# Performance work log

Measured on AMD Instinct MI355X. Metric: run time of the kernel, lower is better.

## Reference

```python
import jax, jax.numpy as jnp
import numpy as np

DECAY = 0.99
EPS = 1e-05
TEMP = 1.0


def setup_inputs() -> dict:
    key = jax.random.key(0)
    k1, k2, k3 = jax.random.split(key, 3)
    B, T, D, C = 64, 512, 256, 1024
    x = jax.random.normal(k1, (B, T, D), dtype=jnp.float32)
    embed = jax.random.normal(k2, (1, C, D), dtype=jnp.float32)
    embed_avg = jax.random.normal(k3, (1, C, D), dtype=jnp.float32)
    cluster_size = jnp.ones((1, C), dtype=jnp.float32)
    return {"x": x, "embed": embed, "embed_avg": embed_avg, "cluster_size": cluster_size}


def reference(x, embed, embed_avg, cluster_size):
    B, T, D = x.shape
    H, C, _ = embed.shape  # H = num_codebooks = 1
    flatten = x.reshape(H, B * T, D)  # pack_one 'h * d'
    e = jax.lax.stop_gradient(embed)  # learnable_codebook = False

    dist = (2.0 * jnp.einsum('hnd,hcd->hnc', flatten, e)
            - jnp.sum(flatten * flatten, axis=-1, keepdims=True)
            - jnp.sum(e * e, axis=-1)[:, None, :])  # [h, N, C]

    # gumbel_sample: deterministic argmax + straight-through one-hot
    embed_ind = jnp.argmax(dist, axis=-1)  # [h, N]
    probs = jax.nn.softmax(dist / TEMP, axis=-1)
    hard = jax.nn.one_hot(embed_ind, C, dtype=dist.dtype)
    embed_onehot = probs + jax.lax.stop_gradient(hard - probs)  # [h, N, C]

    # quantize via onehot matmul (training path)
    quantize = jnp.einsum('hnc,hcd->hnd', embed_onehot, e).reshape(B, T, D)

    # EMA codebook update
    cs_new = DECAY * cluster_size + (1.0 - DECAY) * embed_onehot.sum(axis=1)  # [h, C]
    embed_sum = jnp.einsum('hnd,hnc->hcd', flatten, embed_onehot)  # [h, C, D]
    ea_new = DECAY * embed_avg + (1.0 - DECAY) * embed_sum
    n = jnp.sum(cs_new, axis=-1, keepdims=True)
    cs_smoothed = (cs_new + EPS) / (n + C * EPS) * n  # laplace smoothing * n
    embed_norm = ea_new / cs_smoothed[..., None]  # new codebook [h, C, D]

    return (quantize, embed_ind.reshape(B, T), embed_norm, cs_new)
```

## Files before the change

### kernel.cpp

```cpp
#include <hip/hip_runtime.h>
#include <cstdint>

#define DECAY 0.99f
#define OMD   0.01f
#define EPSV  1e-5f

constexpr int N_PTS   = 32768;
constexpr int D_DIM   = 256;
constexpr int C_CODES = 1024;
constexpr int KPACK   = 768;

constexpr int PG = 4;
constexpr int PK = 8;
constexpr int LCAP = 8192;

typedef _Float16 half8  __attribute__((ext_vector_type(8)));
typedef _Float16 half4v __attribute__((ext_vector_type(4)));
typedef float    floatx4 __attribute__((ext_vector_type(4)));

constexpr size_t WS_ENORM = 0;
constexpr size_t WS_CSSUM = 1024;
constexpr size_t WS_PCNT  = 2048;
constexpr size_t WS_CAND  = 8192;
constexpr size_t WS_A16   = WS_CAND + 1048576;
constexpr size_t WS_B16   = WS_A16 + 12582912;
constexpr size_t WS_TOTAL_FLOATS = WS_B16 + 393216;

__device__ __forceinline__ void async_copy16(const void* g, void* s) {
    __builtin_amdgcn_global_load_lds(
        (const __attribute__((address_space(1))) unsigned int*)(uintptr_t)g,
        (__attribute__((address_space(3))) unsigned int*)(uintptr_t)s, 16, 0, 0);
}

__global__ __launch_bounds__(256) void vq_prep_x(const float* __restrict__ X,
                                                 _Float16* __restrict__ A) {
    int i = blockIdx.x * 256 + threadIdx.x;
    int n = i >> 6, kq = (i & 63) * 4;
    float4 v = reinterpret_cast<const float4*>(X)[i];
    _Float16 h0 = (_Float16)v.x, h1 = (_Float16)v.y, h2 = (_Float16)v.z, h3 = (_Float16)v.w;
    _Float16 l0 = (_Float16)(v.x - (float)h0), l1 = (_Float16)(v.y - (float)h1);
    _Float16 l2 = (_Float16)(v.z - (float)h2), l3 = (_Float16)(v.w - (float)h3);
    half4v hi = {h0, h1, h2, h3};
    half4v lo = {l0, l1, l2, l3};
    _Float16* row = A + (size_t)n * KPACK;
    *reinterpret_cast<half4v*>(row + kq)       = hi;
    *reinterpret_cast<half4v*>(row + 256 + kq) = hi;
    *reinterpret_cast<half4v*>(row + 512 + kq) = lo;
}

__global__ __launch_bounds__(256) void vq_prep_e(const float* __restrict__ E,
                                                 _Float16* __restrict__ B) {
    int i = blockIdx.x * 256 + threadIdx.x;
    int c = i >> 6, kq = (i & 63) * 4;
    float4 v = reinterpret_cast<const float4*>(E)[i];
    _Float16 h0 = (_Float16)v.x, h1 = (_Float16)v.y, h2 = (_Float16)v.z, h3 = (_Float16)v.w;
    _Float16 l0 = (_Float16)(v.x - (float)h0), l1 = (_Float16)(v.y - (float)h1);
    _Float16 l2 = (_Float16)(v.z - (float)h2), l3 = (_Float16)(v.w - (float)h3);
    half4v hi = {h0, h1, h2, h3};
    half4v lo = {l0, l1, l2, l3};
    _Float16* row = B + (size_t)c * KPACK;
    *reinterpret_cast<half4v*>(row + kq)       = hi;
    *reinterpret_cast<half4v*>(row + 256 + kq) = lo;
    *reinterpret_cast<half4v*>(row + 512 + kq) = hi;
}

__global__ __launch_bounds__(256) void vq_enorm(const float* __restrict__ E,
                                                float* __restrict__ enorm) {
    int c    = blockIdx.x * 4 + (threadIdx.x >> 6);
    int lane = threadIdx.x & 63;
    float4 v = reinterpret_cast<const float4*>(E)[c * 64 + lane];
    float s  = v.x * v.x + v.y * v.y + v.z * v.z + v.w * v.w;
#pragma unroll
    for (int off = 32; off > 0; off >>= 1) s += __shfl_down(s, off, 64);
    if (lane == 0) enorm[c] = s;
}

__global__ __launch_bounds__(1024) void vq_cssum(const float* __restrict__ cs_in,
                                                 float* __restrict__ out) {
    __shared__ float red[1024];
    int t = threadIdx.x;
    red[t] = cs_in[t];
    __syncthreads();
    for (int s = 512; s > 0; s >>= 1) {
        if (t < s) red[t] += red[t + s];
        __syncthreads();
    }
    if (t == 0) out[0] = red[0];
}

__global__ __launch_bounds__(256, 2) void vq_gemm(
    const _Float16* __restrict__ A, const _Float16* __restrict__ B,
    const float* __restrict__ enorm, float2* __restrict__ cand) {
    __shared__ _Float16 As[128 * 64];
    __shared__ _Float16 Bs[128 * 64];

    const int L      = blockIdx.x;
    const int within = L >> 3;
    const int ct     = within & 7;
    const int rt     = (L & 7) | ((within >> 3) << 3);
    const int n0     = rt * 128;
    const int cb0    = ct * 128;

    const int tid = threadIdx.x;
    const int w   = tid >> 6;
    const int l   = tid & 63;

    const int srow = l >> 3;
    const int sq   = (l & 7) ^ srow;

    floatx4 acc[4][4] = {};

    for (int k0 = 0; k0 < KPACK; k0 += 64) {
        __syncthreads();
#pragma unroll
        for (int t = 0; t < 4; ++t) {
            int rr = w * 32 + t * 8;
            const _Float16* ga = A + (size_t)(n0 + rr + srow) * KPACK + k0 + sq * 8;
            async_copy16(ga, &As[rr * 64]);
            const _Float16* gb = B + (size_t)(cb0 + rr + srow) * KPACK + k0 + sq * 8;
            async_copy16(gb, &Bs[rr * 64]);
        }
        __syncthreads();
#pragma unroll
        for (int kk = 0; kk < 2; ++kk) {
            half8 af[4], bf[4];
            int qa = kk * 4 + (l >> 4);
#pragma unroll
            for (int i = 0; i < 4; ++i) {
                int row  = (w & 1) * 64 + 16 * i + (l & 15);
                af[i] = *reinterpret_cast<const half8*>(&As[row * 64 + (qa ^ (row & 7)) * 8]);
                int crow = (w >> 1) * 64 + 16 * i + (l & 15);
                bf[i] = *reinterpret_cast<const half8*>(&Bs[crow * 64 + (qa ^ (crow & 7)) * 8]);
            }
#pragma unroll
            for (int i = 0; i < 4; ++i)
#pragma unroll
                for (int j = 0; j < 4; ++j)
                    acc[i][j] = __builtin_amdgcn_mfma_f32_16x16x32_f16(af[i], bf[j], acc[i][j], 0, 0, 0);
        }
    }

    const int colbase = cb0 + (w >> 1) * 64 + (l & 15);
    float en[4];
#pragma unroll
    for (int j = 0; j < 4; ++j) en[j] = enorm[colbase + 16 * j];

#pragma unroll
    for (int i = 0; i < 4; ++i) {
#pragma unroll
        for (int reg = 0; reg < 4; ++reg) {
            float bv = -3.4e38f;
            int   bi = 0x7fffffff;
#pragma unroll
            for (int j = 0; j < 4; ++j) {
                float v = 2.0f * acc[i][j][reg] - en[j];
                int   c = colbase + 16 * j;
                if (v > bv || (v == bv && c < bi)) { bv = v; bi = c; }
            }
#pragma unroll
            for (int s = 1; s < 16; s <<= 1) {
                float ov = __shfl_xor(bv, s, 64);
                int   oi = __shfl_xor(bi, s, 64);
                if (ov > bv || (ov == bv && oi < bi)) { bv = ov; bi = oi; }
            }
            if ((l & 15) == 0) {
                int row = n0 + (w & 1) * 64 + 16 * i + (l >> 4) * 4 + reg;
                cand[(size_t)row * 16 + ct * 2 + (w >> 1)] = make_float2(bv, (float)bi);
            }
        }
    }
}

__global__ __launch_bounds__(256) void vq_merge3(
    const float2* __restrict__ cand, const float* __restrict__ E,
    float* __restrict__ quant, float* __restrict__ indout) {
    __shared__ int rowsel[64];
    const int tid = threadIdx.x;
    const int n0  = blockIdx.x * 64;

    if (tid < 64) {
        int r = n0 + tid;
        float bv = -3.4e38f;
        int   bi = 0x7fffffff;
#pragma unroll
        for (int t = 0; t < 16; ++t) {
            float2 cv = cand[(size_t)r * 16 + t];
            int ci = (int)cv.y;
            if (cv.x > bv || (cv.x == bv && ci < bi)) { bv = cv.x; bi = ci; }
        }
        bi &= (C_CODES - 1);
        rowsel[tid] = bi;
        indout[r]   = (float)bi;
    }
    __syncthreads();

    const float4* E4 = reinterpret_cast<const float4*>(E);
    float4*       Q4 = reinterpret_cast<float4*>(quant);
    const int lane = tid & 63;
#pragma unroll
    for (int it = 0; it < 16; ++it) {
        int r   = (tid >> 6) + 4 * it;
        int idx = rowsel[r];
        Q4[(n0 + r) * 64 + lane] = E4[idx * 64 + lane];
    }
}

__global__ __launch_bounds__(256) void vq_part(
    const float* __restrict__ X, const float* __restrict__ indf,
    float* __restrict__ P, int* __restrict__ pcnt) {
    __shared__ int list[LCAP];
    __shared__ int cnt[PK];
    __shared__ int lcnt;
    const int cg = blockIdx.x;
    const int g  = blockIdx.y;
    const int t  = threadIdx.x;
    if (t == 0) lcnt = 0;
    if (t < PK) cnt[t] = 0;
    __syncthreads();

    const float4* I4 = reinterpret_cast<const float4*>(indf);
    float4 v[8];
#pragma unroll
    for (int j = 0; j < 8; ++j)
        v[j] = I4[g * 2048 + j * 256 + t];

#pragma unroll
    for (int j = 0; j < 8; ++j) {
        int base = (g * 2048 + j * 256 + t) * 4;
        int k0 = (int)v[j].x, k1 = (int)v[j].y, k2 = (int)v[j].z, k3 = (int)v[j].w;
        if ((k0 >> 3) == cg) { int p = atomicAdd(&lcnt, 1); atomicAdd(&cnt[k0 & 7], 1); if (p < LCAP) list[p] = ((base + 0) << 3) | (k0 & 7); }
        if ((k1 >> 3) == cg) { int p = atomicAdd(&lcnt, 1); atomicAdd(&cnt[k1 & 7], 1); if (p < LCAP) list[p] = ((base + 1) << 3) | (k1 & 7); }
        if ((k2 >> 3) == cg) { int p = atomicAdd(&lcnt, 1); atomicAdd(&cnt[k2 & 7], 1); if (p < LCAP) list[p] = ((base + 2) << 3) | (k2 & 7); }
        if ((k3 >> 3) == cg) { int p = atomicAdd(&lcnt, 1); atomicAdd(&cnt[k3 & 7], 1); if (p < LCAP) list[p] = ((base + 3) << 3) | (k3 & 7); }
    }
    __syncthreads();

    int m = lcnt; if (m > LCAP) m = LCAP;
    float acc[PK] = {0, 0, 0, 0, 0, 0, 0, 0};
    int r = 0;
    for (; r + 8 <= m; r += 8) {
        int e[8];
        float val[8];
#pragma unroll
        for (int q = 0; q < 8; ++q) e[q] = list[r + q];
#pragma unroll
        for (int q = 0; q < 8; ++q) val[q] = X[(size_t)(e[q] >> 3) * D_DIM + t];
#pragma unroll
        for (int q = 0; q < 8; ++q) {
            int k = e[q] & 7;
#pragma unroll
            for (int kk = 0; kk < PK; ++kk) acc[kk] += (k == kk) ? val[q] : 0.0f;
        }
    }
    for (; r < m; ++r) {
        int e = list[r];
        float val = X[(size_t)(e >> 3) * D_DIM + t];
        int k = e & 7;
#pragma unroll
        for (int kk = 0; kk < PK; ++kk) acc[kk] += (k == kk) ? val : 0.0f;
    }

#pragma unroll
    for (int kk = 0; kk < PK; ++kk)
        P[((size_t)g * C_CODES + cg * PK + kk) * D_DIM + t] = acc[kk];
    if (t < PK) pcnt[g * C_CODES + cg * PK + t] = cnt[t];
}

__global__ __launch_bounds__(256) void vq_comb(
    const float* __restrict__ P, const int* __restrict__ pcnt,
    const float* __restrict__ ea, const float* __restrict__ cs_in,
    const float* __restrict__ cs_sum,
    float* __restrict__ emb_norm, float* __restrict__ cs_out) {
    const int c = blockIdx.x;
    const int t = threadIdx.x;
    float s = 0.0f;
#pragma unroll
    for (int g = 0; g < PG; ++g)
        s += P[((size_t)g * C_CODES + c) * D_DIM + t];
    int total = pcnt[c] + pcnt[C_CODES + c] + pcnt[2 * C_CODES + c] + pcnt[3 * C_CODES + c];
    float cs    = DECAY * cs_in[c] + OMD * (float)total;
    float ntot  = DECAY * cs_sum[0] + OMD * (float)N_PTS;
    float denom = (cs + EPSV) / (ntot + (float)C_CODES * EPSV) * ntot;
    emb_norm[(size_t)c * D_DIM + t] =
        (DECAY * ea[(size_t)c * D_DIM + t] + OMD * s) / denom;
    if (t == 0) cs_out[c] = cs;
}

__global__ __launch_bounds__(256) void vq_main_fb(
    const float* __restrict__ X, const float* __restrict__ E,
    const float* __restrict__ enorm,
    float* __restrict__ quant, float* __restrict__ indout,
    float* __restrict__ counts, float* __restrict__ esum) {
    constexpr int BN = 64, BC = 64, BK = 32, PADR = 68;
    __shared__ float As[BK * PADR];
    __shared__ float Bs[BK * PADR];
    __shared__ float redv[BN * 16];
    __shared__ int   redi[BN * 16];
    __shared__ int   rowsel[BN];

    const int tid = threadIdx.x;
    const int n0  = blockIdx.x * BN;
    const int tr  = tid >> 4;
    const int tc  = tid & 15;
    const int sr  = tid >> 2;
    const int sk  = tid & 3;

    const float4* X4 = reinterpret_cast<const float4*>(X);
    const float4* E4 = reinterpret_cast<const float4*>(E);

    float best[4];
    int   bidx[4];
#pragma unroll
    for (int i = 0; i < 4; i++) { best[i] = -3.4e38f; bidx[i] = 0; }

    for (int c0 = 0; c0 < C_CODES; c0 += BC) {
        float acc[4][4] = {};
        for (int k0 = 0; k0 < D_DIM; k0 += BK) {
            __syncthreads();
#pragma unroll
            for (int it = 0; it < 2; ++it) {
                int   k4 = sk + 4 * it;
                float4 av = X4[(n0 + sr) * 64 + (k0 >> 2) + k4];
                float4 bv = E4[(c0 + sr) * 64 + (k0 >> 2) + k4];
                int kk = k4 * 4;
                As[(kk + 0) * PADR + sr] = av.x;
                As[(kk + 1) * PADR + sr] = av.y;
                As[(kk + 2) * PADR + sr] = av.z;
                As[(kk + 3) * PADR + sr] = av.w;
                Bs[(kk + 0) * PADR + sr] = bv.x;
                Bs[(kk + 1) * PADR + sr] = bv.y;
                Bs[(kk + 2) * PADR + sr] = bv.z;
                Bs[(kk + 3) * PADR + sr] = bv.w;
            }
            __syncthreads();
#pragma unroll
            for (int k = 0; k < BK; ++k) {
                float4 a = *reinterpret_cast<const float4*>(&As[k * PADR + 4 * tr]);
                float4 b = *reinterpret_cast<const float4*>(&Bs[k * PADR + 4 * tc]);
                acc[0][0] += a.x * b.x; acc[0][1] += a.x * b.y;
                acc[0][2] += a.x * b.z; acc[0][3] += a.x * b.w;
                acc[1][0] += a.y * b.x; acc[1][1] += a.y * b.y;
                acc[1][2] += a.y * b.z; acc[1][3] += a.y * b.w;
                acc[2][0] += a.z * b.x; acc[2][1] += a.z * b.y;
                acc[2][2] += a.z * b.z; acc[2][3] += a.z * b.w;
                acc[3][0] += a.w * b.x; acc[3][1] += a.w * b.y;
                acc[3][2] += a.w * b.z; acc[3][3] += a.w * b.w;
            }
        }
        float4 en = *reinterpret_cast<const float4*>(&enorm[c0 + 4 * tc]);
        float enj[4] = {en.x, en.y, en.z, en.w};
#pragma unroll
        for (int i = 0; i < 4; i++)
#pragma unroll
            for (int j = 0; j < 4; j++) {
                float v = 2.0f * acc[i][j] - enj[j];
                int   c = c0 + 4 * tc + j;
                if (v > best[i]) { best[i] = v; bidx[i] = c; }
            }
    }

    __syncthreads();
#pragma unroll
    for (int i = 0; i < 4; i++) {
        redv[(4 * tr + i) * 16 + tc] = best[i];
        redi[(4 * tr + i) * 16 + tc] = bidx[i];
    }
    __syncthreads();
    if (tid < BN) {
        float bv = redv[tid * 16];
        int   bi = redi[tid * 16];
        for (int t = 1; t < 16; t++) {
            float v  = redv[tid * 16 + t];
            int   id = redi[tid * 16 + t];
            if (v > bv || (v == bv && id < bi)) { bv = v; bi = id; }
        }
        rowsel[tid] = bi;
        indout[n0 + tid] = (float)bi;
        unsafeAtomicAdd(&counts[bi], 1.0f);
    }
    __syncthreads();

    float4*   Q4   = reinterpret_cast<float4*>(quant);
    const int lane = tid & 63;
#pragma unroll
    for (int it = 0; it < 16; ++it) {
        int r   = (tid >> 6) + 4 * it;
        int idx = rowsel[r];
        float4 ev = E4[idx * 64 + lane];
        Q4[(n0 + r) * 64 + lane] = ev;
        float4 xv = X4[(n0 + r) * 64 + lane];
        float* dst = &esum[idx * D_DIM + lane * 4];
        unsafeAtomicAdd(dst + 0, xv.x);
        unsafeAtomicAdd(dst + 1, xv.y);
        unsafeAtomicAdd(dst + 2, xv.z);
        unsafeAtomicAdd(dst + 3, xv.w);
    }
}

__global__ __launch_bounds__(1024) void vq_fin1(const float* __restrict__ cs_in,
                                                const float* __restrict__ counts,
                                                float* __restrict__ cs_out,
                                                float* __restrict__ denom) {
    __shared__ float red[1024];
    int   c  = threadIdx.x;
    float cs = DECAY * cs_in[c] + OMD * counts[c];
    cs_out[c] = cs;
    red[c]    = cs;
    __syncthreads();
    for (int s = 512; s > 0; s >>= 1) {
        if (c < s) red[c] += red[c + s];
        __syncthreads();
    }
    float ntot = red[0];
    denom[c] = (cs + EPSV) / (ntot + (float)C_CODES * EPSV) * ntot;
}

__global__ __launch_bounds__(256) void vq_fin2(const float* __restrict__ ea,
                                               const float* __restrict__ esum,
                                               const float* __restrict__ denom,
                                               float* __restrict__ out) {
    int i = blockIdx.x * 256 + threadIdx.x;
    int c = i >> 6;
    float4 a = reinterpret_cast<const float4*>(ea)[i];
    float4 s = reinterpret_cast<const float4*>(esum)[i];
    float  d = denom[c];
    float4 o;
    o.x = (DECAY * a.x + OMD * s.x) / d;
    o.y = (DECAY * a.y + OMD * s.y) / d;
    o.z = (DECAY * a.z + OMD * s.z) / d;
    o.w = (DECAY * a.w + OMD * s.w) / d;
    reinterpret_cast<float4*>(out)[i] = o;
}

extern "C" void kernel_launch(void* const* d_in, const int* in_sizes, int n_in,
                              void* d_out, int out_size, void* d_ws, size_t ws_size,
                              hipStream_t stream) {
    const float* x            = (const float*)d_in[0];
    const float* embed        = (const float*)d_in[1];
    const float* embed_avg    = (const float*)d_in[2];
    const float* cluster_size = (const float*)d_in[3];

    float* out      = (float*)d_out;
    float* quant    = out;
    float* ind      = out + (size_t)N_PTS * D_DIM;
    float* emb_norm = ind + N_PTS;
    float* cs_out   = emb_norm + (size_t)C_CODES * D_DIM;

    float* ws    = (float*)d_ws;
    float* enorm = ws + WS_ENORM;

    vq_enorm<<<C_CODES / 4, 256, 0, stream>>>(embed, enorm);

    if (ws_size >= WS_TOTAL_FLOATS * sizeof(float)) {
        float*    cssum = ws + WS_CSSUM;
        int*      pcnt  = (int*)(ws + WS_PCNT);
        float2*   cand  = (float2*)(ws + WS_CAND);
        float*    P     = ws + WS_CAND;
        _Float16* A16   = (_Float16*)(ws + WS_A16);
        _Float16* B16   = (_Float16*)(ws + WS_B16);

        vq_cssum<<<1, 1024, 0, stream>>>(cluster_size, cssum);
        vq_prep_x<<<N_PTS * 64 / 256, 256, 0, stream>>>(x, A16);
        vq_prep_e<<<C_CODES * 64 / 256, 256, 0, stream>>>(embed, B16);
        vq_gemm<<<2048, 256, 0, stream>>>(A16, B16, enorm, cand);
        vq_merge3<<<N_PTS / 64, 256, 0, stream>>>(cand, embed, quant, ind);
        vq_part<<<dim3(C_CODES / PK, PG), 256, 0, stream>>>(x, ind, P, pcnt);
        vq_comb<<<C_CODES, 256, 0, stream>>>(P, pcnt, embed_avg, cluster_size, cssum,
                                             emb_norm, cs_out);
    } else {
        float* countsf = ws + WS_CAND;
        float* esum    = ws + WS_CAND + 1024;
        float* denom   = ws + WS_A16;
        hipMemsetAsync(countsf, 0, (1024 + (size_t)C_CODES * D_DIM) * sizeof(float), stream);
        vq_main_fb<<<N_PTS / 64, 256, 0, stream>>>(x, embed, enorm, quant, ind, countsf, esum);
        vq_fin1<<<1, 1024, 0, stream>>>(cluster_size, countsf, cs_out, denom);
        vq_fin2<<<(C_CODES * D_DIM / 4) / 256, 256, 0, stream>>>(embed_avg, esum, denom, emb_norm);
    }
}
```

Before: 218.1 us.

## Store split-fp16 operands once and form cross terms in-register; fuse small prep kernels

The packed A/B rows shrink from three 256-wide segments (hi,hi,lo / hi,lo,hi) to two (hi,lo). The GEMM now loads hi and lo tiles separately into LDS and issues three MFMAs per fragment pair (hh, hl, lh), so it reads less global memory and the prep kernel writes less for the same compensated product. The codebook-norm computation moves into vq_prep_e and the cluster-size sum moves into vq_comb, removing two kernel launches. In exchange the GEMM uses twice the LDS and more registers per block, which may reduce occupancy under the (256,2) launch bound, and every vq_comb block now recomputes the 1024-element sum redundantly.

```diff
diff --git a/kernel.cpp b/kernel.cpp
--- a/kernel.cpp
+++ b/kernel.cpp
@@ -8,7 +8,7 @@
 constexpr int N_PTS   = 32768;
 constexpr int D_DIM   = 256;
 constexpr int C_CODES = 1024;
-constexpr int KPACK   = 768;
+constexpr int KPACK   = 512;
 
 constexpr int PG = 4;
 constexpr int PK = 8;
@@ -19,12 +19,11 @@
 typedef float    floatx4 __attribute__((ext_vector_type(4)));
 
 constexpr size_t WS_ENORM = 0;
-constexpr size_t WS_CSSUM = 1024;
 constexpr size_t WS_PCNT  = 2048;
 constexpr size_t WS_CAND  = 8192;
 constexpr size_t WS_A16   = WS_CAND + 1048576;
-constexpr size_t WS_B16   = WS_A16 + 12582912;
-constexpr size_t WS_TOTAL_FLOATS = WS_B16 + 393216;
+constexpr size_t WS_B16   = WS_A16 + 8388608;
+constexpr size_t WS_TOTAL_FLOATS = WS_B16 + 262144;
 
 __device__ __forceinline__ void async_copy16(const void* g, void* s) {
     __builtin_amdgcn_global_load_lds(
@@ -44,12 +43,12 @@
     half4v lo = {l0, l1, l2, l3};
     _Float16* row = A + (size_t)n * KPACK;
     *reinterpret_cast<half4v*>(row + kq)       = hi;
-    *reinterpret_cast<half4v*>(row + 256 + kq) = hi;
-    *reinterpret_cast<half4v*>(row + 512 + kq) = lo;
+    *reinterpret_cast<half4v*>(row + 256 + kq) = lo;
 }
 
 __global__ __launch_bounds__(256) void vq_prep_e(const float* __restrict__ E,
-                                                 _Float16* __restrict__ B) {
+                                                 _Float16* __restrict__ B,
+                                                 float* __restrict__ enorm) {
     int i = blockIdx.x * 256 + threadIdx.x;
     int c = i >> 6, kq = (i & 63) * 4;
     float4 v = reinterpret_cast<const float4*>(E)[i];
@@ -61,7 +60,10 @@
     _Float16* row = B + (size_t)c * KPACK;
     *reinterpret_cast<half4v*>(row + kq)       = hi;
     *reinterpret_cast<half4v*>(row + 256 + kq) = lo;
-    *reinterpret_cast<half4v*>(row + 512 + kq) = hi;
+    float s = v.x * v.x + v.y * v.y + v.z * v.z + v.w * v.w;
+#pragma unroll
+    for (int off = 32; off > 0; off >>= 1) s += __shfl_down(s, off, 64);
+    if ((threadIdx.x & 63) == 0) enorm[c] = s;
 }
 
 __global__ __launch_bounds__(256) void vq_enorm(const float* __restrict__ E,
@@ -75,24 +77,13 @@
     if (lane == 0) enorm[c] = s;
 }
 
-__global__ __launch_bounds__(1024) void vq_cssum(const float* __restrict__ cs_in,
-                                                 float* __restrict__ out) {
-    __shared__ float red[1024];
-    int t = threadIdx.x;
-    red[t] = cs_in[t];
-    __syncthreads();
-    for (int s = 512; s > 0; s >>= 1) {
-        if (t < s) red[t] += red[t + s];
-        __syncthreads();
-    }
-    if (t == 0) out[0] = red[0];
-}
-
 __global__ __launch_bounds__(256, 2) void vq_gemm(
     const _Float16* __restrict__ A, const _Float16* __restrict__ B,
     const float* __restrict__ enorm, float2* __restrict__ cand) {
-    __shared__ _Float16 As[128 * 64];
-    __shared__ _Float16 Bs[128 * 64];
+    __shared__ _Float16 Ah[128 * 64];
+    __shared__ _Float16 Al[128 * 64];
+    __shared__ _Float16 Bh[128 * 64];
+    __shared__ _Float16 Bl[128 * 64];
 
     const int L      = blockIdx.x;
     const int within = L >> 3;
@@ -110,33 +101,42 @@
 
     floatx4 acc[4][4] = {};
 
-    for (int k0 = 0; k0 < KPACK; k0 += 64) {
+    for (int k0 = 0; k0 < 256; k0 += 64) {
         __syncthreads();
 #pragma unroll
         for (int t = 0; t < 4; ++t) {
             int rr = w * 32 + t * 8;
             const _Float16* ga = A + (size_t)(n0 + rr + srow) * KPACK + k0 + sq * 8;
-            async_copy16(ga, &As[rr * 64]);
+            async_copy16(ga,       &Ah[rr * 64]);
+            async_copy16(ga + 256, &Al[rr * 64]);
             const _Float16* gb = B + (size_t)(cb0 + rr + srow) * KPACK + k0 + sq * 8;
-            async_copy16(gb, &Bs[rr * 64]);
+            async_copy16(gb,       &Bh[rr * 64]);
+            async_copy16(gb + 256, &Bl[rr * 64]);
         }
         __syncthreads();
 #pragma unroll
         for (int kk = 0; kk < 2; ++kk) {
-            half8 af[4], bf[4];
+            half8 ah[4], al4[4], bh[4], bl4[4];
             int qa = kk * 4 + (l >> 4);
 #pragma unroll
             for (int i = 0; i < 4; ++i) {
                 int row  = (w & 1) * 64 + 16 * i + (l & 15);
-                af[i] = *reinterpret_cast<const half8*>(&As[row * 64 + (qa ^ (row & 7)) * 8]);
+                int aoff = row * 64 + (qa ^ (row & 7)) * 8;
+                ah[i]  = *reinterpret_cast<const half8*>(&Ah[aoff]);
+                al4[i] = *reinterpret_cast<const half8*>(&Al[aoff]);
                 int crow = (w >> 1) * 64 + 16 * i + (l & 15);
-                bf[i] = *reinterpret_cast<const half8*>(&Bs[crow * 64 + (qa ^ (crow & 7)) * 8]);
+                int boff = crow * 64 + (qa ^ (crow & 7)) * 8;
+                bh[i]  = *reinterpret_cast<const half8*>(&Bh[boff]);
+                bl4[i] = *reinterpret_cast<const half8*>(&Bl[boff]);
             }
 #pragma unroll
             for (int i = 0; i < 4; ++i)
 #pragma unroll
-                for (int j = 0; j < 4; ++j)
-                    acc[i][j] = __builtin_amdgcn_mfma_f32_16x16x32_f16(af[i], bf[j], acc[i][j], 0, 0, 0);
+                for (int j = 0; j < 4; ++j) {
+                    acc[i][j] = __builtin_amdgcn_mfma_f32_16x16x32_f16(ah[i],  bh[j],  acc[i][j], 0, 0, 0);
+                    acc[i][j] = __builtin_amdgcn_mfma_f32_16x16x32_f16(ah[i],  bl4[j], acc[i][j], 0, 0, 0);
+                    acc[i][j] = __builtin_amdgcn_mfma_f32_16x16x32_f16(al4[i], bh[j],  acc[i][j], 0, 0, 0);
+                }
         }
     }
 
@@ -269,17 +269,25 @@
 __global__ __launch_bounds__(256) void vq_comb(
     const float* __restrict__ P, const int* __restrict__ pcnt,
     const float* __restrict__ ea, const float* __restrict__ cs_in,
-    const float* __restrict__ cs_sum,
     float* __restrict__ emb_norm, float* __restrict__ cs_out) {
+    __shared__ float red[4];
     const int c = blockIdx.x;
     const int t = threadIdx.x;
+    float ls = cs_in[t] + cs_in[256 + t] + cs_in[512 + t] + cs_in[768 + t];
+#pragma unroll
+    for (int off = 32; off > 0; off >>= 1) ls += __shfl_down(ls, off, 64);
+    if ((t & 63) == 0) red[t >> 6] = ls;
+
     float s = 0.0f;
 #pragma unroll
     for (int g = 0; g < PG; ++g)
         s += P[((size_t)g * C_CODES + c) * D_DIM + t];
     int total = pcnt[c] + pcnt[C_CODES + c] + pcnt[2 * C_CODES + c] + pcnt[3 * C_CODES + c];
+    __syncthreads();
+    float cssum = red[0] + red[1] + red[2] + red[3];
+
     float cs    = DECAY * cs_in[c] + OMD * (float)total;
-    float ntot  = DECAY * cs_sum[0] + OMD * (float)N_PTS;
+    float ntot  = DECAY * cssum + OMD * (float)N_PTS;
     float denom = (cs + EPSV) / (ntot + (float)C_CODES * EPSV) * ntot;
     emb_norm[(size_t)c * D_DIM + t] =
         (DECAY * ea[(size_t)c * D_DIM + t] + OMD * s) / denom;
@@ -449,28 +457,25 @@
     float* ws    = (float*)d_ws;
     float* enorm = ws + WS_ENORM;
 
-    vq_enorm<<<C_CODES / 4, 256, 0, stream>>>(embed, enorm);
-
     if (ws_size >= WS_TOTAL_FLOATS * sizeof(float)) {
-        float*    cssum = ws + WS_CSSUM;
         int*      pcnt  = (int*)(ws + WS_PCNT);
         float2*   cand  = (float2*)(ws + WS_CAND);
         float*    P     = ws + WS_CAND;
         _Float16* A16   = (_Float16*)(ws + WS_A16);
         _Float16* B16   = (_Float16*)(ws + WS_B16);
 
-        vq_cssum<<<1, 1024, 0, stream>>>(cluster_size, cssum);
         vq_prep_x<<<N_PTS * 64 / 256, 256, 0, stream>>>(x, A16);
-        vq_prep_e<<<C_CODES * 64 / 256, 256, 0, stream>>>(embed, B16);
+        vq_prep_e<<<C_CODES * 64 / 256, 256, 0, stream>>>(embed, B16, enorm);
         vq_gemm<<<2048, 256, 0, stream>>>(A16, B16, enorm, cand);
         vq_merge3<<<N_PTS / 64, 256, 0, stream>>>(cand, embed, quant, ind);
         vq_part<<<dim3(C_CODES / PK, PG), 256, 0, stream>>>(x, ind, P, pcnt);
-        vq_comb<<<C_CODES, 256, 0, stream>>>(P, pcnt, embed_avg, cluster_size, cssum,
+        vq_comb<<<C_CODES, 256, 0, stream>>>(P, pcnt, embed_avg, cluster_size,
                                              emb_norm, cs_out);
     } else {
         float* countsf = ws + WS_CAND;
         float* esum    = ws + WS_CAND + 1024;
         float* denom   = ws + WS_A16;
+        vq_enorm<<<C_CODES / 4, 256, 0, stream>>>(embed, enorm);
         hipMemsetAsync(countsf, 0, (1024 + (size_t)C_CODES * D_DIM) * sizeof(float), stream);
         vq_main_fb<<<N_PTS / 64, 256, 0, stream>>>(x, embed, enorm, quant, ind, countsf, esum);
         vq_fin1<<<1, 1024, 0, stream>>>(cluster_size, countsf, cs_out, denom);
```

New measurement: 221.5 us. Within noise of the previous version (+1.6%).
